# Kernel optimization log

Measured on AMD Instinct MI355X. Metric: run time of the kernel, lower is better.

Reference implementation:

```python
import jax, jax.numpy as jnp
import numpy as np


def setup_inputs() -> dict:
    key = jax.random.key(0)
    k1, k2, k3, k4 = jax.random.split(key, 4)
    latent = jax.random.normal(k1, (4, 8192, 1024), dtype=jnp.float32)
    W = jax.random.normal(k2, (1024, 3), dtype=jnp.float32) * (1.0 / np.sqrt(1024))
    b = jax.random.normal(k3, (3,), dtype=jnp.float32) * 0.02
    noise = jax.random.normal(k4, (4, 8192, 3), dtype=jnp.float32)
    return {"latent": latent, "W": W, "b": b, "noise": noise, "steps": 50}


def reference(latent, W, b, noise, steps):
    # target = proj(latent): [B, N, 3]
    target = jnp.einsum("bnd,dk->bnk", latent, W) + b
    # reverse diffusion: for t in reversed(range(steps)):
    #   alpha = (t+1)/steps; x = alpha*x + (1-alpha)*target
    alphas = jnp.arange(steps, 0, -1, dtype=jnp.float32) / steps  # alpha_t for t=steps-1..0

    def step(x, a):
        return a * x + (1.0 - a) * target, None

    x, _ = jax.lax.scan(step, noise, alphas)
    return x
```

## Files before the change

### kernel.cpp

```cpp
#include <hip/hip_runtime.h>


constexpr int D = 1024;

__global__ __launch_bounds__(256) void diff_init_kernel(
    const float* __restrict__ latent,
    const float* __restrict__ W,
    const float* __restrict__ bvec,
    const float* __restrict__ noise,
    const int*   __restrict__ steps_p,
    float*       __restrict__ out,
    int rows)
{
    const int lane   = threadIdx.x & 63;
    const int wave   = blockIdx.x * (blockDim.x >> 6) + (threadIdx.x >> 6);
    const int nwaves = gridDim.x * (blockDim.x >> 6);

    const int steps = steps_p[0];
    float P = 1.0f;
    for (int t = steps; t >= 1; --t) P *= (float)t / (float)steps;
    const float Q = 1.0f - P;

    float w[4][12];
    #pragma unroll
    for (int it = 0; it < 4; ++it) {
        const int idx = it * 64 + lane;
        const float4* wp = (const float4*)(W + (size_t)idx * 12);
        float4 wa = wp[0], wb = wp[1], wc = wp[2];
        w[it][0] = wa.x; w[it][1]  = wa.y; w[it][2]  = wa.z; w[it][3]  = wa.w;
        w[it][4] = wb.x; w[it][5]  = wb.y; w[it][6]  = wb.z; w[it][7]  = wb.w;
        w[it][8] = wc.x; w[it][9]  = wc.y; w[it][10] = wc.z; w[it][11] = wc.w;
    }

    const float bb = (lane < 3) ? bvec[lane] : 0.0f;

    for (int row = wave; row < rows; row += nwaves) {
        const float4* lrow = (const float4*)(latent + (size_t)row * D);
        float a0 = 0.0f, a1 = 0.0f, a2 = 0.0f;
        #pragma unroll
        for (int it = 0; it < 4; ++it) {
            float4 lv = lrow[it * 64 + lane];
            a0 = fmaf(lv.x, w[it][0], a0);
            a1 = fmaf(lv.x, w[it][1], a1);
            a2 = fmaf(lv.x, w[it][2], a2);
            a0 = fmaf(lv.y, w[it][3], a0);
            a1 = fmaf(lv.y, w[it][4], a1);
            a2 = fmaf(lv.y, w[it][5], a2);
            a0 = fmaf(lv.z, w[it][6], a0);
            a1 = fmaf(lv.z, w[it][7], a1);
            a2 = fmaf(lv.z, w[it][8], a2);
            a0 = fmaf(lv.w, w[it][9],  a0);
            a1 = fmaf(lv.w, w[it][10], a1);
            a2 = fmaf(lv.w, w[it][11], a2);
        }
        #pragma unroll
        for (int m = 32; m >= 1; m >>= 1) {
            a0 += __shfl_xor(a0, m, 64);
            a1 += __shfl_xor(a1, m, 64);
            a2 += __shfl_xor(a2, m, 64);
        }
        if (lane < 3) {
            const float t  = (lane == 0) ? a0 : (lane == 1 ? a1 : a2);
            const float nz = noise[(size_t)row * 3 + lane];
            out[(size_t)row * 3 + lane] = fmaf(P, nz, Q * (t + bb));
        }
    }
}

extern "C" void kernel_launch(void* const* d_in, const int* in_sizes, int n_in,
                              void* d_out, int out_size, void* d_ws, size_t ws_size,
                              hipStream_t stream) {
    const float* latent = (const float*)d_in[0];
    const float* W      = (const float*)d_in[1];
    const float* bvec   = (const float*)d_in[2];
    const float* noise  = (const float*)d_in[3];
    const int*   steps  = (const int*)d_in[4];
    float* out = (float*)d_out;

    const int rows = in_sizes[0] / D;
    const int blocks = 2048;
    diff_init_kernel<<<blocks, 256, 0, stream>>>(latent, W, bvec, noise, steps,
                                                 out, rows);
}
```

Before: 29.53 us.

## Process four rows per wave with batched loads and merged shuffle reduction

Each wave now handles four consecutive rows, issuing all sixteen float4 loads up front so more memory requests are in flight per wave. The grid is sized to the row count instead of using a grid-stride loop. The three-output butterfly reduction is merged so fewer shuffles are needed per row. The cost is higher register pressure from holding sixteen float4 values, which may lower occupancy.

```diff
diff --git a/kernel.cpp b/kernel.cpp
--- a/kernel.cpp
+++ b/kernel.cpp
@@ -12,9 +12,10 @@
     float*       __restrict__ out,
     int rows)
 {
-    const int lane   = threadIdx.x & 63;
-    const int wave   = blockIdx.x * (blockDim.x >> 6) + (threadIdx.x >> 6);
-    const int nwaves = gridDim.x * (blockDim.x >> 6);
+    const int lane = threadIdx.x & 63;
+    const int wave = blockIdx.x * (blockDim.x >> 6) + (threadIdx.x >> 6);
+    const int row0 = wave * 4;
+    if (row0 >= rows) return;
 
     const int steps = steps_p[0];
     float P = 1.0f;
@@ -24,8 +25,7 @@
     float w[4][12];
     #pragma unroll
     for (int it = 0; it < 4; ++it) {
-        const int idx = it * 64 + lane;
-        const float4* wp = (const float4*)(W + (size_t)idx * 12);
+        const float4* wp = (const float4*)(W + (size_t)(it * 64 + lane) * 12);
         float4 wa = wp[0], wb = wp[1], wc = wp[2];
         w[it][0] = wa.x; w[it][1]  = wa.y; w[it][2]  = wa.z; w[it][3]  = wa.w;
         w[it][4] = wb.x; w[it][5]  = wb.y; w[it][6]  = wb.z; w[it][7]  = wb.w;
@@ -34,35 +34,67 @@
 
     const float bb = (lane < 3) ? bvec[lane] : 0.0f;
 
-    for (int row = wave; row < rows; row += nwaves) {
-        const float4* lrow = (const float4*)(latent + (size_t)row * D);
-        float a0 = 0.0f, a1 = 0.0f, a2 = 0.0f;
+    float4 lv[4][4];
+    const bool full = (row0 + 4 <= rows);
+    if (full) {
+        #pragma unroll
+        for (int r = 0; r < 4; ++r) {
+            const float4* lrow = (const float4*)(latent + (size_t)(row0 + r) * D);
+            #pragma unroll
+            for (int it = 0; it < 4; ++it) lv[r][it] = lrow[it * 64 + lane];
+        }
+    } else {
+        #pragma unroll
+        for (int r = 0; r < 4; ++r) {
+            const float4* lrow = (const float4*)(latent + (size_t)(row0 + r) * D);
+            #pragma unroll
+            for (int it = 0; it < 4; ++it)
+                lv[r][it] = (row0 + r < rows) ? lrow[it * 64 + lane]
+                                              : float4{0.f, 0.f, 0.f, 0.f};
+        }
+    }
+
+    float acc[4][3];
+    #pragma unroll
+    for (int r = 0; r < 4; ++r) {
+        float a0 = 0.f, a1 = 0.f, a2 = 0.f;
         #pragma unroll
         for (int it = 0; it < 4; ++it) {
-            float4 lv = lrow[it * 64 + lane];
-            a0 = fmaf(lv.x, w[it][0], a0);
-            a1 = fmaf(lv.x, w[it][1], a1);
-            a2 = fmaf(lv.x, w[it][2], a2);
-            a0 = fmaf(lv.y, w[it][3], a0);
-            a1 = fmaf(lv.y, w[it][4], a1);
-            a2 = fmaf(lv.y, w[it][5], a2);
-            a0 = fmaf(lv.z, w[it][6], a0);
-            a1 = fmaf(lv.z, w[it][7], a1);
-            a2 = fmaf(lv.z, w[it][8], a2);
-            a0 = fmaf(lv.w, w[it][9],  a0);
-            a1 = fmaf(lv.w, w[it][10], a1);
-            a2 = fmaf(lv.w, w[it][11], a2);
+            float4 lvv = lv[r][it];
+            a0 = fmaf(lvv.x, w[it][0], a0);
+            a1 = fmaf(lvv.x, w[it][1], a1);
+            a2 = fmaf(lvv.x, w[it][2], a2);
+            a0 = fmaf(lvv.y, w[it][3], a0);
+            a1 = fmaf(lvv.y, w[it][4], a1);
+            a2 = fmaf(lvv.y, w[it][5], a2);
+            a0 = fmaf(lvv.z, w[it][6], a0);
+            a1 = fmaf(lvv.z, w[it][7], a1);
+            a2 = fmaf(lvv.z, w[it][8], a2);
+            a0 = fmaf(lvv.w, w[it][9],  a0);
+            a1 = fmaf(lvv.w, w[it][10], a1);
+            a2 = fmaf(lvv.w, w[it][11], a2);
         }
-        #pragma unroll
-        for (int m = 32; m >= 1; m >>= 1) {
-            a0 += __shfl_xor(a0, m, 64);
-            a1 += __shfl_xor(a1, m, 64);
-            a2 += __shfl_xor(a2, m, 64);
-        }
-        if (lane < 3) {
-            const float t  = (lane == 0) ? a0 : (lane == 1 ? a1 : a2);
+        acc[r][0] = a0; acc[r][1] = a1; acc[r][2] = a2;
+    }
+
+    #pragma unroll
+    for (int r = 0; r < 4; ++r) {
+        float a = acc[r][0], b = acc[r][1], c = acc[r][2];
+        float keep = (lane & 1) ? b : a;
+        float send = (lane & 1) ? a : b;
+        float v = keep + __shfl_xor(send, 1, 64);
+        c += __shfl_xor(c, 1, 64);
+        float keep2 = (lane & 2) ? c : v;
+        float send2 = (lane & 2) ? v : c;
+        float u = keep2 + __shfl_xor(send2, 2, 64);
+        u += __shfl_xor(u, 4, 64);
+        u += __shfl_xor(u, 8, 64);
+        u += __shfl_xor(u, 16, 64);
+        u += __shfl_xor(u, 32, 64);
+        const int row = row0 + r;
+        if (lane < 3 && row < rows) {
             const float nz = noise[(size_t)row * 3 + lane];
-            out[(size_t)row * 3 + lane] = fmaf(P, nz, Q * (t + bb));
+            out[(size_t)row * 3 + lane] = fmaf(P, nz, Q * (u + bb));
         }
     }
 }
@@ -77,8 +109,9 @@
     const int*   steps  = (const int*)d_in[4];
     float* out = (float*)d_out;
 
-    const int rows = in_sizes[0] / D;
-    const int blocks = 2048;
+    const int rows   = in_sizes[0] / D;
+    const int waves  = (rows + 3) / 4;
+    const int blocks = (waves + 3) / 4;
     diff_init_kernel<<<blocks, 256, 0, stream>>>(latent, W, bvec, noise, steps,
                                                  out, rows);
 }
```

Result: slower. 33.56 us (+13.6%).

## Compute latent projection with bf16 MFMA and LDS split-K reduction

Applied to the files above, without the earlier changes.

Replaces the per-wave FMA dot product and shuffle reduction with 16x16x32 bf16 MFMA instructions. Each block handles 16 rows, its four waves split K four ways, and partial results are combined through shared memory. The kernel is dominated by streaming 128 MB of latent, so compute savings may matter little. Converting inputs to bf16 adds rounding error, and most of the MFMA output columns are wasted because only 3 are real.

```diff
diff --git a/kernel.cpp b/kernel.cpp
--- a/kernel.cpp
+++ b/kernel.cpp
@@ -1,9 +1,19 @@
 #include <hip/hip_runtime.h>
+#include <hip/hip_bf16.h>
 
+
+typedef float f32x4  __attribute__((ext_vector_type(4)));
+typedef short bf16x8 __attribute__((ext_vector_type(8)));
 
 constexpr int D = 1024;
 
-__global__ __launch_bounds__(256) void diff_init_kernel(
+static __device__ __forceinline__ short f2bf(float f) {
+    union { __hip_bfloat16 h; unsigned short u; } cv;
+    cv.h = __float2bfloat16(f);
+    return (short)cv.u;
+}
+
+__global__ __launch_bounds__(256) void diff_init_mfma(
     const float* __restrict__ latent,
     const float* __restrict__ W,
     const float* __restrict__ bvec,
@@ -12,58 +22,60 @@
     float*       __restrict__ out,
     int rows)
 {
-    const int lane   = threadIdx.x & 63;
-    const int wave   = blockIdx.x * (blockDim.x >> 6) + (threadIdx.x >> 6);
-    const int nwaves = gridDim.x * (blockDim.x >> 6);
+    const int lane = threadIdx.x & 63;
+    const int q    = threadIdx.x >> 6;
+    const int row0 = blockIdx.x * 16;
+
+    const int rc = lane & 15;
+    const int bq = lane >> 4;
+
+    bf16x8 bfrag[8];
+    #pragma unroll
+    for (int i = 0; i < 8; ++i) {
+        const int kb = q * 256 + i * 32 + bq * 8;
+        #pragma unroll
+        for (int j = 0; j < 8; ++j) {
+            const float v = (rc < 3) ? W[(size_t)(kb + j) * 3 + rc] : 0.0f;
+            bfrag[i][j] = f2bf(v);
+        }
+    }
+
+    int arow_i = row0 + rc; if (arow_i > rows - 1) arow_i = rows - 1;
+    const float* arow = latent + (size_t)arow_i * D + q * 256 + bq * 8;
+
+    f32x4 acc = {0.f, 0.f, 0.f, 0.f};
+    #pragma unroll
+    for (int i = 0; i < 8; ++i) {
+        const f32x4* p = (const f32x4*)(arow + i * 32);
+        const f32x4 a0 = p[0], a1 = p[1];
+        bf16x8 af;
+        af[0] = f2bf(a0.x); af[1] = f2bf(a0.y);
+        af[2] = f2bf(a0.z); af[3] = f2bf(a0.w);
+        af[4] = f2bf(a1.x); af[5] = f2bf(a1.y);
+        af[6] = f2bf(a1.z); af[7] = f2bf(a1.w);
+        acc = __builtin_amdgcn_mfma_f32_16x16x32_bf16(af, bfrag[i], acc, 0, 0, 0);
+    }
 
     const int steps = steps_p[0];
     float P = 1.0f;
     for (int t = steps; t >= 1; --t) P *= (float)t / (float)steps;
     const float Q = 1.0f - P;
 
-    float w[4][12];
-    #pragma unroll
-    for (int it = 0; it < 4; ++it) {
-        const int idx = it * 64 + lane;
-        const float4* wp = (const float4*)(W + (size_t)idx * 12);
-        float4 wa = wp[0], wb = wp[1], wc = wp[2];
-        w[it][0] = wa.x; w[it][1]  = wa.y; w[it][2]  = wa.z; w[it][3]  = wa.w;
-        w[it][4] = wb.x; w[it][5]  = wb.y; w[it][6]  = wb.z; w[it][7]  = wb.w;
-        w[it][8] = wc.x; w[it][9]  = wc.y; w[it][10] = wc.z; w[it][11] = wc.w;
-    }
+    __shared__ f32x4 part[4][64];
+    part[q][lane] = acc;
+    __syncthreads();
 
-    const float bb = (lane < 3) ? bvec[lane] : 0.0f;
+    const float* pp = (const float*)part;
+    const float s = pp[(0 * 64 + lane) * 4 + q]
+                  + pp[(1 * 64 + lane) * 4 + q]
+                  + pp[(2 * 64 + lane) * 4 + q]
+                  + pp[(3 * 64 + lane) * 4 + q];
 
-    for (int row = wave; row < rows; row += nwaves) {
-        const float4* lrow = (const float4*)(latent + (size_t)row * D);
-        float a0 = 0.0f, a1 = 0.0f, a2 = 0.0f;
-        #pragma unroll
-        for (int it = 0; it < 4; ++it) {
-            float4 lv = lrow[it * 64 + lane];
-            a0 = fmaf(lv.x, w[it][0], a0);
-            a1 = fmaf(lv.x, w[it][1], a1);
-            a2 = fmaf(lv.x, w[it][2], a2);
-            a0 = fmaf(lv.y, w[it][3], a0);
-            a1 = fmaf(lv.y, w[it][4], a1);
-            a2 = fmaf(lv.y, w[it][5], a2);
-            a0 = fmaf(lv.z, w[it][6], a0);
-            a1 = fmaf(lv.z, w[it][7], a1);
-            a2 = fmaf(lv.z, w[it][8], a2);
-            a0 = fmaf(lv.w, w[it][9],  a0);
-            a1 = fmaf(lv.w, w[it][10], a1);
-            a2 = fmaf(lv.w, w[it][11], a2);
-        }
-        #pragma unroll
-        for (int m = 32; m >= 1; m >>= 1) {
-            a0 += __shfl_xor(a0, m, 64);
-            a1 += __shfl_xor(a1, m, 64);
-            a2 += __shfl_xor(a2, m, 64);
-        }
-        if (lane < 3) {
-            const float t  = (lane == 0) ? a0 : (lane == 1 ? a1 : a2);
-            const float nz = noise[(size_t)row * 3 + lane];
-            out[(size_t)row * 3 + lane] = fmaf(P, nz, Q * (t + bb));
-        }
+    const int col = rc;
+    const int row = row0 + bq * 4 + q;
+    if (col < 3 && row < rows) {
+        const size_t idx = (size_t)row * 3 + col;
+        out[idx] = fmaf(P, noise[idx], Q * (s + bvec[col]));
     }
 }
 
@@ -77,8 +89,8 @@
     const int*   steps  = (const int*)d_in[4];
     float* out = (float*)d_out;
 
-    const int rows = in_sizes[0] / D;
-    const int blocks = 2048;
-    diff_init_kernel<<<blocks, 256, 0, stream>>>(latent, W, bvec, noise, steps,
-                                                 out, rows);
+    const int rows   = in_sizes[0] / D;
+    const int blocks = (rows + 15) / 16;
+    diff_init_mfma<<<blocks, 256, 0, stream>>>(latent, W, bvec, noise, steps,
+                                               out, rows);
 }
```

Result: slower. 41.56 us (+40.7%).
